# Performance work log

Measured on AMD Instinct MI355X. Metric: run time of the kernel, lower is better.

The kernel has to match this reference:

```python
import jax, jax.numpy as jnp
import numpy as np

B, C, J, T = 32, 128, 24, 128
Q, K = 6, 1024
EPS = 1e-10


def setup_inputs() -> dict:
    key = jax.random.key(0)
    k1, k2 = jax.random.split(key)
    x = jax.random.normal(k1, (B, C, J, T), dtype=jnp.float32)
    codebooks = jax.random.normal(k2, (Q, K, C), dtype=jnp.float32)
    return {"x": x, "codebooks": codebooks}


def reference(x, codebooks):
    """Residual VQ over 2D joint-temporal tokens.
    x: (B, C, J, T); codebooks: (Q, K, C).
    Returns (quantized_out (B,C,J,T), all_indices (B,J,T,Q), loss scalar, perplexity scalar).
    """
    b, c, j, t = x.shape
    q, k, _ = codebooks.shape
    # preprocess: (B, C, J, T) -> (B*J*T, C)
    xf = jnp.transpose(x, (0, 2, 3, 1)).reshape(-1, c)
    m = xf.shape[0]

    def step(carry, codebook):
        residual, q_out = carry
        # squared L2 distances (M, K)
        d = (jnp.sum(residual * residual, axis=-1, keepdims=True)
             - 2.0 * (residual @ codebook.T)
             + jnp.sum(codebook * codebook, axis=-1))
        idx = jnp.argmin(d, axis=-1)                       # (M,)
        xd = codebook[idx]                                 # dequantize (M, C)
        # commitment loss: mse(x, x_d.detach())
        loss = jnp.mean((residual - jax.lax.stop_gradient(xd)) ** 2)
        # perplexity from code usage histogram
        counts = jax.ops.segment_sum(jnp.ones((m,), xf.dtype), idx, num_segments=k)
        p = counts / m
        perp = jnp.exp(-jnp.sum(p * jnp.log(p + EPS)))
        # straight-through estimator
        quant = residual + jax.lax.stop_gradient(xd - residual)
        # residual = residual - quantized.detach(); quantized_out += quantized
        new_res = residual - jax.lax.stop_gradient(quant)
        return (new_res, q_out + quant), (idx, loss, perp)

    init = (xf, jnp.zeros_like(xf))
    (_, q_out), (idxs, losses, perps) = jax.lax.scan(step, init, codebooks)

    quantized_out = jnp.transpose(q_out.reshape(b, j, t, c), (0, 3, 1, 2))
    all_indices = jnp.transpose(idxs, (1, 0)).reshape(b, j, t, q)
    return quantized_out, all_indices, jnp.mean(losses), jnp.mean(perps)
```

## Files before the change

kernel.cpp:

```cpp
#include <hip/hip_runtime.h>

typedef __attribute__((ext_vector_type(8))) short short8v;
typedef __attribute__((ext_vector_type(4))) float f32x4;

#define B_ 32
#define C_ 128
#define J_ 24
#define T_ 128
#define Q_ 6
#define K_ 1024
#define JT (J_*T_)
#define M_ (B_*JT)
#define NBLK 768

#define OUT_QUANT 0
#define OUT_IDX   12582912
#define OUT_LOSS  13172736
#define OUT_PERP  13172737

#define TAU 0.02f

__device__ __forceinline__ unsigned short f2bf(float f) {
    unsigned int u = __float_as_uint(f);
    u = (u + 0x7FFFu + ((u >> 16) & 1u)) >> 16;
    return (unsigned short)u;
}
__device__ __forceinline__ float bf2f(unsigned short h) {
    return __uint_as_float(((unsigned int)h) << 16);
}

__device__ __forceinline__ void gload16(const void* g, void* lds) {
    __builtin_amdgcn_global_load_lds(
        (const __attribute__((address_space(1))) void*)g,
        (__attribute__((address_space(3))) void*)lds, 16, 0, 0);
}

__global__ __launch_bounds__(256) void c2_kernel(const float* __restrict__ cb,
                                                 float* __restrict__ c2) {
    int wave = (blockIdx.x * blockDim.x + threadIdx.x) >> 6;
    int lane = threadIdx.x & 63;
    if (wave >= Q_ * K_) return;
    const float2 v = reinterpret_cast<const float2*>(cb + (size_t)wave * C_)[lane];
    float s = v.x * v.x + v.y * v.y;
    #pragma unroll
    for (int off = 32; off; off >>= 1) s += __shfl_down(s, off, 64);
    if (lane == 0) c2[wave] = s;
}

__global__ __launch_bounds__(256) void cbtile_kernel(const float* __restrict__ cb,
                                                     unsigned short* __restrict__ cbt) {
    int i = blockIdx.x * 256 + threadIdx.x;
    if (i >= Q_ * 32 * 1024) return;
    int q = i >> 15;
    int rem = i & 32767;
    int tau = rem >> 10;
    int slot = rem & 1023;
    int part = slot >> 9;
    int ks = (slot >> 7) & 3;
    int nt = (slot >> 6) & 1;
    int r6 = slot & 63;
    int a = (r6 >> 4) & 3;
    int b3 = (r6 >> 3) & 1;
    int low3 = r6 & 7;
    int c4 = (b3 << 3) | (low3 ^ a);
    int code = tau * 32 + nt * 16 + c4;
    const float* src = cb + ((size_t)q * K_ + code) * C_ + ks * 32 + a * 8;
    short8v v;
    #pragma unroll
    for (int j = 0; j < 8; ++j) {
        float f = src[j];
        unsigned short hh = f2bf(f);
        v[j] = (part == 0) ? (short)hh : (short)f2bf(f - bf2f(hh));
    }
    *(short8v*)(cbt + (size_t)i * 8) = v;
}

__global__ __launch_bounds__(256) void transpose_kernel(const float* __restrict__ x,
                                                        float* __restrict__ res) {
    __shared__ float tile[32][33];
    const int tx = threadIdx.x & 31, ty = threadIdx.x >> 5;
    const int jt0 = blockIdx.x * 32;
    const int c0 = blockIdx.y * 32;
    const int b = blockIdx.z;
    const float* xb = x + ((size_t)b * C_ + c0) * JT + jt0;
    #pragma unroll
    for (int i = 0; i < 4; ++i) {
        int cc = ty + 8 * i;
        tile[cc][tx] = xb[(size_t)cc * JT + tx];
    }
    __syncthreads();
    float* rb = res + ((size_t)b * JT + jt0) * C_ + c0;
    #pragma unroll
    for (int i = 0; i < 4; ++i) {
        int jj = ty + 8 * i;
        rb[(size_t)jj * C_ + tx] = tile[tx][jj];
    }
}

__global__ __launch_bounds__(256, 2) void vq_fused_kernel(
        float* __restrict__ res,
        const float* __restrict__ cb,
        const unsigned short* __restrict__ cbt,
        const float* __restrict__ c2g,
        int* __restrict__ idxws, int* __restrict__ counts,
        float* __restrict__ partials) {
    __shared__ __attribute__((aligned(16))) unsigned short bsA[8192];
    __shared__ __attribute__((aligned(16))) unsigned short bsB[8192];
    __shared__ __attribute__((aligned(16))) unsigned short bsC[8192];
    __shared__ int idx_lds[128];
    __shared__ int nflag[4];
    __shared__ int flagl[4][32];
    __shared__ float wsum[4];
    __shared__ __attribute__((aligned(16))) float rowbuf[4][128];

    const int t = threadIdx.x;
    const int w = t >> 6, l = t & 63;
    const int la = l >> 4;
    const int lc = l & 15;
    const int rowbase = blockIdx.x * 128 + w * 32;
    const int lb = la * 256 + (l & 8) * 16 + (((l & 7) ^ la) * 16);

    float rres[64];
    #pragma unroll
    for (int mf = 0; mf < 2; ++mf) {
        const float* ap = res + (size_t)(rowbase + mf * 16 + lc) * C_ + la * 8;
        #pragma unroll
        for (int ks = 0; ks < 4; ++ks) {
            float4 f0 = *(const float4*)(ap + ks * 32);
            float4 f1 = *(const float4*)(ap + ks * 32 + 4);
            rres[mf * 32 + ks * 8 + 0] = f0.x; rres[mf * 32 + ks * 8 + 1] = f0.y;
            rres[mf * 32 + ks * 8 + 2] = f0.z; rres[mf * 32 + ks * 8 + 3] = f0.w;
            rres[mf * 32 + ks * 8 + 4] = f1.x; rres[mf * 32 + ks * 8 + 5] = f1.y;
            rres[mf * 32 + ks * 8 + 6] = f1.z; rres[mf * 32 + ks * 8 + 7] = f1.w;
        }
    }

#define STAGE(base_, tau_, buf_) { \
        const unsigned short* sp = (base_) + (size_t)(tau_) * 8192 + w * 2048 + l * 8; \
        char* dp = ((char*)(buf_)) + w * 4096; \
        gload16(sp, dp); \
        gload16(sp + 512, dp + 1024); \
        gload16(sp + 1024, dp + 2048); \
        gload16(sp + 1536, dp + 3072); \
    }

    for (int q = 0; q < Q_; ++q) {
        const int qk0 = q * K_;
        const unsigned short* cbase = cbt + (size_t)q * (32 * 8192);
        if (l == 0) nflag[w] = 0;

        short8v ah[2][4], al[2][4];
        #pragma unroll
        for (int mf = 0; mf < 2; ++mf) {
            #pragma unroll
            for (int ks = 0; ks < 4; ++ks) {
                short8v vh, vl;
                #pragma unroll
                for (int j = 0; j < 8; ++j) {
                    float v = rres[mf * 32 + ks * 8 + j];
                    unsigned short hh = f2bf(v);
                    vh[j] = (short)hh;
                    vl[j] = (short)f2bf(v - bf2f(hh));
                }
                ah[mf][ks] = vh;
                al[mf][ks] = vl;
            }
        }

        float bd[2][4], bd2[2][4];
        int bi[2][4];
        #pragma unroll
        for (int mf = 0; mf < 2; ++mf)
            #pragma unroll
            for (int rg = 0; rg < 4; ++rg) {
                bd[mf][rg] = 3.4e38f; bd2[mf][rg] = 3.4e38f; bi[mf][rg] = 0;
            }

        STAGE(cbase, 0, bsA)
        STAGE(cbase, 1, bsB)
        asm volatile("s_waitcnt vmcnt(0)" ::: "memory");
        __builtin_amdgcn_s_barrier();

        const char* bcur = (const char*)bsA;
        const char* bnx1 = (const char*)bsB;
        const char* bnx2 = (const char*)bsC;

        for (int tau = 0; tau < 32; ++tau) {
            const float c2v0 = c2g[qk0 + tau * 32 + lc];
            const float c2v1 = c2g[qk0 + tau * 32 + 16 + lc];
            if (tau < 30) STAGE(cbase, tau + 2, (void*)bnx2)

            #pragma unroll
            for (int nt = 0; nt < 2; ++nt) {
                const int code = tau * 32 + nt * 16 + lc;
                const float c2v = nt ? c2v1 : c2v0;
                f32x4 aA0 = {0.f, 0.f, 0.f, 0.f}, aM0 = aA0, aA1 = aA0, aM1 = aA0;
                #pragma unroll
                for (int ks = 0; ks < 4; ++ks) {
                    const char* bb = bcur + ks * 2048 + nt * 1024 + lb;
                    const short8v bh = *(const short8v*)(bb);
                    const short8v bl = *(const short8v*)(bb + 8192);
                    aA0 = __builtin_amdgcn_mfma_f32_16x16x32_bf16(ah[0][ks], bh, aA0, 0, 0, 0);
                    aM0 = __builtin_amdgcn_mfma_f32_16x16x32_bf16(al[0][ks], bh, aM0, 0, 0, 0);
                    aM0 = __builtin_amdgcn_mfma_f32_16x16x32_bf16(ah[0][ks], bl, aM0, 0, 0, 0);
                    aA1 = __builtin_amdgcn_mfma_f32_16x16x32_bf16(ah[1][ks], bh, aA1, 0, 0, 0);
                    aM1 = __builtin_amdgcn_mfma_f32_16x16x32_bf16(al[1][ks], bh, aM1, 0, 0, 0);
                    aM1 = __builtin_amdgcn_mfma_f32_16x16x32_bf16(ah[1][ks], bl, aM1, 0, 0, 0);
                }
#define UPD(A, Mv, mf, rg) { \
                float s = A[rg] + Mv[rg]; \
                float d = fmaf(-2.f, s, c2v); \
                bool lt = d < bd[mf][rg]; \
                bd2[mf][rg] = lt ? bd[mf][rg] : fminf(bd2[mf][rg], d); \
                bd[mf][rg] = lt ? d : bd[mf][rg]; \
                bi[mf][rg] = lt ? code : bi[mf][rg]; }
                UPD(aA0, aM0, 0, 0) UPD(aA0, aM0, 0, 1) UPD(aA0, aM0, 0, 2) UPD(aA0, aM0, 0, 3)
                UPD(aA1, aM1, 1, 0) UPD(aA1, aM1, 1, 1) UPD(aA1, aM1, 1, 2) UPD(aA1, aM1, 1, 3)
#undef UPD
            }

            if (tau < 30) {
                asm volatile("s_waitcnt vmcnt(4)" ::: "memory");
            } else {
                asm volatile("s_waitcnt vmcnt(0)" ::: "memory");
            }
            __builtin_amdgcn_s_barrier();
            const char* tmp = bcur; bcur = bnx1; bnx1 = bnx2; bnx2 = tmp;
        }

        #pragma unroll
        for (int mf = 0; mf < 2; ++mf) {
            #pragma unroll
            for (int rg = 0; rg < 4; ++rg) {
                float d1 = bd[mf][rg], d2 = bd2[mf][rg];
                int i1 = bi[mf][rg];
                #pragma unroll
                for (int off = 1; off < 16; off <<= 1) {
                    float od1 = __shfl_xor(d1, off);
                    float od2 = __shfl_xor(d2, off);
                    int oi1 = __shfl_xor(i1, off);
                    float nd2 = fminf(fminf(d2, od2), fmaxf(d1, od1));
                    if (od1 < d1 || (od1 == d1 && oi1 < i1)) { d1 = od1; i1 = oi1; }
                    d2 = nd2;
                }
                if (lc == 0) {
                    const int rr = mf * 16 + la * 4 + rg;
                    idx_lds[w * 32 + rr] = i1;
                    if (d2 - d1 < TAU) {
                        int p = atomicAdd(&nflag[w], 1);
                        flagl[w][p] = rr;
                    }
                }
            }
        }

        {
            const int nf = nflag[w];
            for (int f = 0; f < nf; ++f) {
                const int rr = flagl[w][f];
                const int mfr = rr >> 4, r16 = rr & 15;
                if (lc == r16) {
                    #pragma unroll
                    for (int ks = 0; ks < 4; ++ks) {
                        #pragma unroll
                        for (int j = 0; j < 8; ++j)
                            rowbuf[w][la * 8 + ks * 32 + j] =
                                (mfr == 0) ? rres[ks * 8 + j] : rres[32 + ks * 8 + j];
                    }
                }
                asm volatile("s_waitcnt lgkmcnt(0)" ::: "memory");
                __builtin_amdgcn_sched_barrier(0);
                const float4* rf4 = (const float4*)&rowbuf[w][0];
                double bdd = 1e300;
                int bk = 0;
                for (int kk = 0; kk < 16; ++kk) {
                    const int k = l + kk * 64;
                    const float4* bp4 = (const float4*)(cb + ((size_t)qk0 + k) * C_);
                    double s = 0.0;
                    for (int c4 = 0; c4 < 32; ++c4) {
                        float4 bv = bp4[c4];
                        float4 rv = rf4[c4];
                        double d0 = (double)rv.x - (double)bv.x; s = fma(d0, d0, s);
                        double d1 = (double)rv.y - (double)bv.y; s = fma(d1, d1, s);
                        double d2 = (double)rv.z - (double)bv.z; s = fma(d2, d2, s);
                        double d3 = (double)rv.w - (double)bv.w; s = fma(d3, d3, s);
                    }
                    if (s < bdd || (s == bdd && k < bk)) { bdd = s; bk = k; }
                }
                #pragma unroll
                for (int off = 1; off < 64; off <<= 1) {
                    double od = __shfl_xor(bdd, off);
                    int ok = __shfl_xor(bk, off);
                    if (od < bdd || (od == bdd && ok < bk)) { bdd = od; bk = ok; }
                }
                if (l == 0) idx_lds[w * 32 + rr] = bk;
                asm volatile("s_waitcnt lgkmcnt(0)" ::: "memory");
            }
        }

        if (l < 16) {
            const int k0 = idx_lds[w * 32 + l];
            const int k1 = idx_lds[w * 32 + 16 + l];
            idxws[(size_t)q * M_ + rowbase + l] = k0;
            idxws[(size_t)q * M_ + rowbase + 16 + l] = k1;
            atomicAdd(&counts[qk0 + k0], 1);
            atomicAdd(&counts[qk0 + k1], 1);
        }

        float sq = 0.f;
        #pragma unroll
        for (int mf = 0; mf < 2; ++mf) {
            const int k = idx_lds[w * 32 + mf * 16 + lc];
            const float* cbr = cb + ((size_t)qk0 + k) * C_ + la * 8;
            #pragma unroll
            for (int ks = 0; ks < 4; ++ks) {
                float4 cv0 = *(const float4*)(cbr + ks * 32);
                float4 cv1 = *(const float4*)(cbr + ks * 32 + 4);
                float cvv[8] = {cv0.x, cv0.y, cv0.z, cv0.w, cv1.x, cv1.y, cv1.z, cv1.w};
                #pragma unroll
                for (int j = 0; j < 8; ++j) {
                    float rv = rres[mf * 32 + ks * 8 + j];
                    float cvj = cvv[j];
                    float dd = rv - cvj;
                    sq += dd * dd;
                    rres[mf * 32 + ks * 8 + j] = rv - (rv + (cvj - rv));
                }
            }
        }
        #pragma unroll
        for (int off = 32; off; off >>= 1) sq += __shfl_down(sq, off, 64);
        if (l == 0) wsum[w] = sq;
        __syncthreads();
        if (t == 0) partials[q * NBLK + blockIdx.x] = wsum[0] + wsum[1] + wsum[2] + wsum[3];
        __syncthreads();
    }

    #pragma unroll
    for (int mf = 0; mf < 2; ++mf) {
        float* ap = res + (size_t)(rowbase + mf * 16 + lc) * C_ + la * 8;
        #pragma unroll
        for (int ks = 0; ks < 4; ++ks) {
            float4 f0 = *(const float4*)(ap + ks * 32);
            float4 f1 = *(const float4*)(ap + ks * 32 + 4);
            float4 o0, o1;
            o0.x = f0.x - rres[mf * 32 + ks * 8 + 0];
            o0.y = f0.y - rres[mf * 32 + ks * 8 + 1];
            o0.z = f0.z - rres[mf * 32 + ks * 8 + 2];
            o0.w = f0.w - rres[mf * 32 + ks * 8 + 3];
            o1.x = f1.x - rres[mf * 32 + ks * 8 + 4];
            o1.y = f1.y - rres[mf * 32 + ks * 8 + 5];
            o1.z = f1.z - rres[mf * 32 + ks * 8 + 6];
            o1.w = f1.w - rres[mf * 32 + ks * 8 + 7];
            *(float4*)(ap + ks * 32) = o0;
            *(float4*)(ap + ks * 32 + 4) = o1;
        }
    }
#undef STAGE
}

__global__ __launch_bounds__(256) void scalars_kernel(const float* __restrict__ partials,
                                                      const int* __restrict__ counts,
                                                      float* __restrict__ out) {
    __shared__ float red[256];
    const int t = threadIdx.x;
    float loss_acc = 0.f, perp_acc = 0.f;
    for (int q = 0; q < Q_; ++q) {
        float s = 0.f;
        for (int i = t; i < NBLK; i += 256) s += partials[q * NBLK + i];
        red[t] = s;
        __syncthreads();
        for (int o = 128; o; o >>= 1) {
            if (t < o) red[t] += red[t + o];
            __syncthreads();
        }
        if (t == 0) loss_acc += red[0] / (float)(M_ * C_);
        __syncthreads();
    }
    for (int q = 0; q < Q_; ++q) {
        float s = 0.f;
        for (int k = t; k < K_; k += 256) {
            float p = (float)counts[q * K_ + k] / (float)M_;
            s += p * logf(p + 1e-10f);
        }
        red[t] = s;
        __syncthreads();
        for (int o = 128; o; o >>= 1) {
            if (t < o) red[t] += red[t + o];
            __syncthreads();
        }
        if (t == 0) perp_acc += expf(-red[0]);
        __syncthreads();
    }
    if (t == 0) {
        out[OUT_LOSS] = loss_acc / (float)Q_;
        out[OUT_PERP] = perp_acc / (float)Q_;
    }
}

__global__ __launch_bounds__(256) void finalt_kernel(const float* __restrict__ qout,
                                                     float* __restrict__ out) {
    __shared__ float tile[32][33];
    const int tx = threadIdx.x & 31, ty = threadIdx.x >> 5;
    const int jt0 = blockIdx.x * 32;
    const int c0 = blockIdx.y * 32;
    const int b = blockIdx.z;
    const float* qb = qout + ((size_t)b * JT + jt0) * C_ + c0;
    #pragma unroll
    for (int i = 0; i < 4; ++i) {
        int jj = ty + 8 * i;
        tile[jj][tx] = qb[(size_t)jj * C_ + tx];
    }
    __syncthreads();
    float* ob = out + ((size_t)b * C_ + c0) * JT + jt0;
    #pragma unroll
    for (int i = 0; i < 4; ++i) {
        int cc = ty + 8 * i;
        ob[(size_t)cc * JT + tx] = tile[tx][cc];
    }
}

__global__ __launch_bounds__(256) void idxout_kernel(const int* __restrict__ idxin,
                                                     float* __restrict__ out) {
    int f = blockIdx.x * 256 + threadIdx.x;
    if (f >= M_ * Q_) return;
    int m = f / Q_;
    int q = f - m * Q_;
    out[f] = (float)idxin[q * M_ + m];
}

extern "C" void kernel_launch(void* const* d_in, const int* in_sizes, int n_in,
                              void* d_out, int out_size, void* d_ws, size_t ws_size,
                              hipStream_t stream) {
    const float* x = (const float*)d_in[0];
    const float* cb = (const float*)d_in[1];
    float* out = (float*)d_out;
    char* ws = (char*)d_ws;

    float* res = (float*)ws;
    int* idxws = (int*)(ws + 50331648);
    float* c2 = (float*)(ws + 52690944);
    int* counts = (int*)(ws + 52715520);
    float* partials = (float*)(ws + 52740096);
    unsigned short* cbt = (unsigned short*)(ws + 52758528);

    hipMemsetAsync(counts, 0, Q_ * K_ * sizeof(int), stream);
    c2_kernel<<<1536, 256, 0, stream>>>(cb, c2);
    cbtile_kernel<<<768, 256, 0, stream>>>(cb, cbt);
    transpose_kernel<<<dim3(96, 4, 32), 256, 0, stream>>>(x, res);
    vq_fused_kernel<<<NBLK, 256, 0, stream>>>(res, cb, cbt, c2, idxws, counts, partials);
    scalars_kernel<<<1, 256, 0, stream>>>(partials, counts, out);
    finalt_kernel<<<dim3(96, 4, 32), 256, 0, stream>>>(res, out);
    idxout_kernel<<<2304, 256, 0, stream>>>(idxws, out + OUT_IDX);
}
```

Baseline: 870.2 us.

## Deepen codebook staging to four LDS buffers and cache code norms in LDS

The triple-buffered codebook pipeline becomes a four-slot ring with three tiles in flight. The wait and barrier move to the top of each iteration, so each new load is issued only after the barrier confirms the target slot is free. Per-code squared norms are preloaded into LDS once per quantizer step instead of being read from global memory every tile, and MFMA sections get raised wave priority via s_setprio. This raises LDS use per block (an extra 16KB for the fourth slot plus 4KB for norms), which could reduce occupancy under the 2-blocks-per-CU launch bound.

After: 875.1 us. Within noise of the previous version (+0.6%).

```diff
diff --git a/kernel.cpp b/kernel.cpp
--- a/kernel.cpp
+++ b/kernel.cpp
@@ -104,9 +104,8 @@
         const float* __restrict__ c2g,
         int* __restrict__ idxws, int* __restrict__ counts,
         float* __restrict__ partials) {
-    __shared__ __attribute__((aligned(16))) unsigned short bsA[8192];
-    __shared__ __attribute__((aligned(16))) unsigned short bsB[8192];
-    __shared__ __attribute__((aligned(16))) unsigned short bsC[8192];
+    __shared__ __attribute__((aligned(16))) unsigned short bs[4][8192];
+    __shared__ float c2_lds[1024];
     __shared__ int idx_lds[128];
     __shared__ int nflag[4];
     __shared__ int flagl[4][32];
@@ -135,9 +134,9 @@
         }
     }
 
-#define STAGE(base_, tau_, buf_) { \
+#define STAGE(base_, tau_, slot_) { \
         const unsigned short* sp = (base_) + (size_t)(tau_) * 8192 + w * 2048 + l * 8; \
-        char* dp = ((char*)(buf_)) + w * 4096; \
+        char* dp = ((char*)bs[slot_]) + w * 4096; \
         gload16(sp, dp); \
         gload16(sp + 512, dp + 1024); \
         gload16(sp + 1024, dp + 2048); \
@@ -148,6 +147,17 @@
         const int qk0 = q * K_;
         const unsigned short* cbase = cbt + (size_t)q * (32 * 8192);
         if (l == 0) nflag[w] = 0;
+
+        float c2tmp[4];
+        #pragma unroll
+        for (int i = 0; i < 4; ++i) c2tmp[i] = c2g[qk0 + t + 256 * i];
+
+        STAGE(cbase, 0, 0)
+        STAGE(cbase, 1, 1)
+        STAGE(cbase, 2, 2)
+
+        #pragma unroll
+        for (int i = 0; i < 4; ++i) c2_lds[t + 256 * i] = c2tmp[i];
 
         short8v ah[2][4], al[2][4];
         #pragma unroll
@@ -176,28 +186,32 @@
                 bd[mf][rg] = 3.4e38f; bd2[mf][rg] = 3.4e38f; bi[mf][rg] = 0;
             }
 
-        STAGE(cbase, 0, bsA)
-        STAGE(cbase, 1, bsB)
-        asm volatile("s_waitcnt vmcnt(0)" ::: "memory");
-        __builtin_amdgcn_s_barrier();
-
-        const char* bcur = (const char*)bsA;
-        const char* bnx1 = (const char*)bsB;
-        const char* bnx2 = (const char*)bsC;
+        asm volatile("s_waitcnt lgkmcnt(0)" ::: "memory");
 
         for (int tau = 0; tau < 32; ++tau) {
-            const float c2v0 = c2g[qk0 + tau * 32 + lc];
-            const float c2v1 = c2g[qk0 + tau * 32 + 16 + lc];
-            if (tau < 30) STAGE(cbase, tau + 2, (void*)bnx2)
+            if (tau < 30) {
+                asm volatile("s_waitcnt vmcnt(8)" ::: "memory");
+            } else if (tau == 30) {
+                asm volatile("s_waitcnt vmcnt(4)" ::: "memory");
+            } else {
+                asm volatile("s_waitcnt vmcnt(0)" ::: "memory");
+            }
+            __builtin_amdgcn_s_barrier();
+            if (tau < 29) STAGE(cbase, tau + 3, (tau + 3) & 3)
+
+            const char* bufp = (const char*)bs[tau & 3];
+            const float c2v0 = c2_lds[tau * 32 + lc];
+            const float c2v1 = c2_lds[tau * 32 + 16 + lc];
 
             #pragma unroll
             for (int nt = 0; nt < 2; ++nt) {
                 const int code = tau * 32 + nt * 16 + lc;
                 const float c2v = nt ? c2v1 : c2v0;
                 f32x4 aA0 = {0.f, 0.f, 0.f, 0.f}, aM0 = aA0, aA1 = aA0, aM1 = aA0;
+                __builtin_amdgcn_s_setprio(1);
                 #pragma unroll
                 for (int ks = 0; ks < 4; ++ks) {
-                    const char* bb = bcur + ks * 2048 + nt * 1024 + lb;
+                    const char* bb = bufp + ks * 2048 + nt * 1024 + lb;
                     const short8v bh = *(const short8v*)(bb);
                     const short8v bl = *(const short8v*)(bb + 8192);
                     aA0 = __builtin_amdgcn_mfma_f32_16x16x32_bf16(ah[0][ks], bh, aA0, 0, 0, 0);
@@ -207,6 +221,7 @@
                     aM1 = __builtin_amdgcn_mfma_f32_16x16x32_bf16(al[1][ks], bh, aM1, 0, 0, 0);
                     aM1 = __builtin_amdgcn_mfma_f32_16x16x32_bf16(ah[1][ks], bl, aM1, 0, 0, 0);
                 }
+                __builtin_amdgcn_s_setprio(0);
 #define UPD(A, Mv, mf, rg) { \
                 float s = A[rg] + Mv[rg]; \
                 float d = fmaf(-2.f, s, c2v); \
@@ -218,14 +233,6 @@
                 UPD(aA1, aM1, 1, 0) UPD(aA1, aM1, 1, 1) UPD(aA1, aM1, 1, 2) UPD(aA1, aM1, 1, 3)
 #undef UPD
             }
-
-            if (tau < 30) {
-                asm volatile("s_waitcnt vmcnt(4)" ::: "memory");
-            } else {
-                asm volatile("s_waitcnt vmcnt(0)" ::: "memory");
-            }
-            __builtin_amdgcn_s_barrier();
-            const char* tmp = bcur; bcur = bnx1; bnx1 = bnx2; bnx2 = tmp;
         }
 
         #pragma unroll
```

## Fold codebook norm into MFMA accumulator and track max score instead of distance

Applied to the files above, without the earlier changes.

Each accumulator is seeded with -0.5*||c||^2 and all three split-bf16 MFMA products go into one accumulator, so the argmin becomes an argmax over the score with no separate add/fma epilogue. This halves accumulator registers, which supports raising launch bounds to 3 waves per SIMD. The codebook-norm loads are prefetched one tile ahead and the first two tile stages are issued before the bf16 hi/lo split to overlap latency. The near-tie threshold is halved to match the scaled score, and the argmax update uses fmax-based logic.

After: 780.4 us. 1.12x faster.

```diff
diff --git a/kernel.cpp b/kernel.cpp
--- a/kernel.cpp
+++ b/kernel.cpp
@@ -18,7 +18,7 @@
 #define OUT_LOSS  13172736
 #define OUT_PERP  13172737
 
-#define TAU 0.02f
+#define TAU_S 0.01f
 
 __device__ __forceinline__ unsigned short f2bf(float f) {
     unsigned int u = __float_as_uint(f);
@@ -97,7 +97,7 @@
     }
 }
 
-__global__ __launch_bounds__(256, 2) void vq_fused_kernel(
+__global__ __launch_bounds__(256, 3) void vq_fused_kernel(
         float* __restrict__ res,
         const float* __restrict__ cb,
         const unsigned short* __restrict__ cbt,
@@ -149,6 +149,12 @@
         const unsigned short* cbase = cbt + (size_t)q * (32 * 8192);
         if (l == 0) nflag[w] = 0;
 
+        float c2r0 = c2g[qk0 + lc];
+        float c2r1 = c2g[qk0 + 16 + lc];
+
+        STAGE(cbase, 0, bsA)
+        STAGE(cbase, 1, bsB)
+
         short8v ah[2][4], al[2][4];
         #pragma unroll
         for (int mf = 0; mf < 2; ++mf) {
@@ -167,64 +173,70 @@
             }
         }
 
-        float bd[2][4], bd2[2][4];
+        float bs[2][4], bs2[2][4];
         int bi[2][4];
         #pragma unroll
         for (int mf = 0; mf < 2; ++mf)
             #pragma unroll
             for (int rg = 0; rg < 4; ++rg) {
-                bd[mf][rg] = 3.4e38f; bd2[mf][rg] = 3.4e38f; bi[mf][rg] = 0;
-            }
-
-        STAGE(cbase, 0, bsA)
-        STAGE(cbase, 1, bsB)
-        asm volatile("s_waitcnt vmcnt(0)" ::: "memory");
+                bs[mf][rg] = -3.4e38f; bs2[mf][rg] = -3.4e38f; bi[mf][rg] = 0;
+            }
+
+        asm volatile("s_waitcnt vmcnt(4)" ::: "memory");
         __builtin_amdgcn_s_barrier();
+        float c2n0 = -0.5f * c2r0;
+        float c2n1 = -0.5f * c2r1;
 
         const char* bcur = (const char*)bsA;
         const char* bnx1 = (const char*)bsB;
         const char* bnx2 = (const char*)bsC;
 
         for (int tau = 0; tau < 32; ++tau) {
-            const float c2v0 = c2g[qk0 + tau * 32 + lc];
-            const float c2v1 = c2g[qk0 + tau * 32 + 16 + lc];
+            if (tau < 31) {
+                c2r0 = c2g[qk0 + (tau + 1) * 32 + lc];
+                c2r1 = c2g[qk0 + (tau + 1) * 32 + 16 + lc];
+            }
             if (tau < 30) STAGE(cbase, tau + 2, (void*)bnx2)
 
             #pragma unroll
             for (int nt = 0; nt < 2; ++nt) {
                 const int code = tau * 32 + nt * 16 + lc;
-                const float c2v = nt ? c2v1 : c2v0;
-                f32x4 aA0 = {0.f, 0.f, 0.f, 0.f}, aM0 = aA0, aA1 = aA0, aM1 = aA0;
+                const float cinit = nt ? c2n1 : c2n0;
+                f32x4 acc0 = {cinit, cinit, cinit, cinit};
+                f32x4 acc1 = acc0;
                 #pragma unroll
                 for (int ks = 0; ks < 4; ++ks) {
                     const char* bb = bcur + ks * 2048 + nt * 1024 + lb;
                     const short8v bh = *(const short8v*)(bb);
                     const short8v bl = *(const short8v*)(bb + 8192);
-                    aA0 = __builtin_amdgcn_mfma_f32_16x16x32_bf16(ah[0][ks], bh, aA0, 0, 0, 0);
-                    aM0 = __builtin_amdgcn_mfma_f32_16x16x32_bf16(al[0][ks], bh, aM0, 0, 0, 0);
-                    aM0 = __builtin_amdgcn_mfma_f32_16x16x32_bf16(ah[0][ks], bl, aM0, 0, 0, 0);
-                    aA1 = __builtin_amdgcn_mfma_f32_16x16x32_bf16(ah[1][ks], bh, aA1, 0, 0, 0);
-                    aM1 = __builtin_amdgcn_mfma_f32_16x16x32_bf16(al[1][ks], bh, aM1, 0, 0, 0);
-                    aM1 = __builtin_amdgcn_mfma_f32_16x16x32_bf16(ah[1][ks], bl, aM1, 0, 0, 0);
-                }
-#define UPD(A, Mv, mf, rg) { \
-                float s = A[rg] + Mv[rg]; \
-                float d = fmaf(-2.f, s, c2v); \
-                bool lt = d < bd[mf][rg]; \
-                bd2[mf][rg] = lt ? bd[mf][rg] : fminf(bd2[mf][rg], d); \
-                bd[mf][rg] = lt ? d : bd[mf][rg]; \
-                bi[mf][rg] = lt ? code : bi[mf][rg]; }
-                UPD(aA0, aM0, 0, 0) UPD(aA0, aM0, 0, 1) UPD(aA0, aM0, 0, 2) UPD(aA0, aM0, 0, 3)
-                UPD(aA1, aM1, 1, 0) UPD(aA1, aM1, 1, 1) UPD(aA1, aM1, 1, 2) UPD(aA1, aM1, 1, 3)
+                    acc0 = __builtin_amdgcn_mfma_f32_16x16x32_bf16(ah[0][ks], bh, acc0, 0, 0, 0);
+                    acc0 = __builtin_amdgcn_mfma_f32_16x16x32_bf16(al[0][ks], bh, acc0, 0, 0, 0);
+                    acc0 = __builtin_amdgcn_mfma_f32_16x16x32_bf16(ah[0][ks], bl, acc0, 0, 0, 0);
+                    acc1 = __builtin_amdgcn_mfma_f32_16x16x32_bf16(ah[1][ks], bh, acc1, 0, 0, 0);
+                    acc1 = __builtin_amdgcn_mfma_f32_16x16x32_bf16(al[1][ks], bh, acc1, 0, 0, 0);
+                    acc1 = __builtin_amdgcn_mfma_f32_16x16x32_bf16(ah[1][ks], bl, acc1, 0, 0, 0);
+                }
+#define UPD(A, mf, rg) { \
+                float v = A[rg]; \
+                bs2[mf][rg] = fmaxf(bs2[mf][rg], fminf(bs[mf][rg], v)); \
+                bool gt = v > bs[mf][rg]; \
+                bs[mf][rg] = fmaxf(bs[mf][rg], v); \
+                bi[mf][rg] = gt ? code : bi[mf][rg]; }
+                UPD(acc0, 0, 0) UPD(acc0, 0, 1) UPD(acc0, 0, 2) UPD(acc0, 0, 3)
+                UPD(acc1, 1, 0) UPD(acc1, 1, 1) UPD(acc1, 1, 2) UPD(acc1, 1, 3)
 #undef UPD
             }
 
             if (tau < 30) {
                 asm volatile("s_waitcnt vmcnt(4)" ::: "memory");
+            } else if (tau == 30) {
+                asm volatile("s_waitcnt vmcnt(2)" ::: "memory");
             } else {
                 asm volatile("s_waitcnt vmcnt(0)" ::: "memory");
             }
             __builtin_amdgcn_s_barrier();
+            c2n0 = -0.5f * c2r0;
+            c2n1 = -0.5f * c2r1;
             const char* tmp = bcur; bcur = bnx1; bnx1 = bnx2; bnx2 = tmp;
         }
 
@@ -232,21 +244,21 @@
         for (int mf = 0; mf < 2; ++mf) {
             #pragma unroll
             for (int rg = 0; rg < 4; ++rg) {
-                float d1 = bd[mf][rg], d2 = bd2[mf][rg];
+                float s1 = bs[mf][rg], s2 = bs2[mf][rg];
                 int i1 = bi[mf][rg];
                 #pragma unroll
                 for (int off = 1; off < 16; off <<= 1) {
-                    float od1 = __shfl_xor(d1, off);
-                    float od2 = __shfl_xor(d2, off);
+                    float os1 = __shfl_xor(s1, off);
+                    float os2 = __shfl_xor(s2, off);
                     int oi1 = __shfl_xor(i1, off);
-                    float nd2 = fminf(fminf(d2, od2), fmaxf(d1, od1));
-                    if (od1 < d1 || (od1 == d1 && oi1 < i1)) { d1 = od1; i1 = oi1; }
-                    d2 = nd2;
+                    float ns2 = fmaxf(fmaxf(s2, os2), fminf(s1, os1));
+                    if (os1 > s1 || (os1 == s1 && oi1 < i1)) { s1 = os1; i1 = oi1; }
+                    s2 = ns2;
                 }
                 if (lc == 0) {
                     const int rr = mf * 16 + la * 4 + rg;
                     idx_lds[w * 32 + rr] = i1;
-                    if (d2 - d1 < TAU) {
+                    if (s1 - s2 < TAU_S) {
                         int p = atomicAdd(&nflag[w], 1);
                         flagl[w][p] = rr;
                     }
```
